# Kernel tuning notes

Hardware: AMD Instinct MI355X
Metric: run time of the kernel (lower is better)

## Reference

```python
import jax, jax.numpy as jnp
import numpy as np

VOCAB = 32000
D_IN = 1024      # == 2 * N_OUT so highway uses raw x (k=3 SRU path)
N_OUT = 512      # hidden per direction
N_LAYERS = 4
L, B = 1024, 16


def _sru_bidir_layer(x, W, b, n):
    """x: (L,B,2n), W: (2n, 6n) [dir0: xt,f,r | dir1: xt,f,r], b: (4n,) = [bf(2n), br(2n)]."""
    u = jnp.einsum('lbd,dk->lbk', x, W)  # (L,B,6n)
    bf, br = b[:2 * n], b[2 * n:]
    hs, cs = [], []
    for d, rev in ((0, False), (1, True)):
        ud = u[..., d * 3 * n:(d + 1) * 3 * n]
        xt = ud[..., :n]
        f = jax.nn.sigmoid(ud[..., n:2 * n] + bf[d * n:(d + 1) * n])
        r = jax.nn.sigmoid(ud[..., 2 * n:3 * n] + br[d * n:(d + 1) * n])
        xp = x[..., d * n:(d + 1) * n]  # highway input (k=3 case)

        def step(c, inp):
            xt_t, f_t, r_t, xp_t = inp
            c = f_t * c + (1.0 - f_t) * xt_t
            h = r_t * jnp.tanh(c) + (1.0 - r_t) * xp_t
            return c, h

        c0 = jnp.zeros((x.shape[1], n), x.dtype)
        c_last, h = jax.lax.scan(step, c0, (xt, f, r, xp), reverse=rev)
        hs.append(h)
        cs.append(c_last)
    return jnp.concatenate(hs, -1), jnp.concatenate(cs, -1)


def setup_inputs() -> dict:
    key = jax.random.key(0)
    k1, k2, k3, k4 = jax.random.split(key, 4)
    rnn_input = jax.random.randint(k1, (L, B), 0, VOCAB, dtype=jnp.int32)
    input_lengths = jax.random.randint(k2, (B,), 1, L + 1, dtype=jnp.int32)
    emb = jax.random.normal(k3, (VOCAB, D_IN), dtype=jnp.float32) * 0.05
    scale = 1.0 / np.sqrt(D_IN)
    Ws = jax.random.normal(k4, (N_LAYERS, D_IN, 6 * N_OUT), dtype=jnp.float32) * scale
    bs = jnp.zeros((N_LAYERS, 4 * N_OUT), dtype=jnp.float32)
    return {"rnn_input": rnn_input, "input_lengths": input_lengths,
            "emb": emb, "Ws": Ws, "bs": bs}


def reference(rnn_input, input_lengths, emb, Ws, bs):
    # input_lengths is unused in the original forward (no packing applied to SRU input)
    n = Ws.shape[-1] // 6
    x = emb[rnn_input]  # (L,B,D_IN)
    c_finals = []
    for l in range(Ws.shape[0]):
        x, c = _sru_bidir_layer(x, Ws[l], bs[l], n)
        c_finals.append(c)
    hidden = jnp.stack(c_finals, 0)  # (N_LAYERS, B, 2n)
    return x, hidden
```

## Files before the change

kernel.cpp:

```cpp
#include <hip/hip_runtime.h>
#include <hip/hip_bf16.h>
#include <cmath>

#define L_SEQ  1024
#define BATCH  16
#define NOUT   512
#define DIN    1024
#define NBIG   3072
#define NLAYERS 4
#define NTOK   (L_SEQ * BATCH)
#define NCHAIN 16384
#define SEG    32
#define SEGLEN (L_SEQ / SEG)

typedef __attribute__((ext_vector_type(8))) short bf16x8;
typedef __attribute__((ext_vector_type(4))) float f32x4;

__device__ __forceinline__ unsigned short f2bf(float f) {
    unsigned x = __float_as_uint(f);
    unsigned r = (x + 0x7fffu + ((x >> 16) & 1u)) >> 16;
    return (unsigned short)r;
}
__device__ __forceinline__ float bf2f(unsigned short hv) {
    return __uint_as_float((unsigned)hv << 16);
}
__device__ __forceinline__ float sigmf(float v) {
    return 1.f / (1.f + __expf(-v));
}
__device__ __forceinline__ void async16(const void* g, const void* l) {
    __builtin_amdgcn_global_load_lds(
        (const __attribute__((address_space(1))) unsigned int*)g,
        (__attribute__((address_space(3))) unsigned int*)l, 16, 0, 0);
}

__global__ __launch_bounds__(256)
void transpose_w(const float* __restrict__ Ws, unsigned short* __restrict__ Wt) {
    __shared__ float tile[32][33];
    int l = blockIdx.z;
    const float* W = Ws + (size_t)l * DIN * NBIG;
    unsigned short* Wo = Wt + (size_t)l * NBIG * DIN;
    int n0 = blockIdx.x * 32, k0 = blockIdx.y * 32;
    int tx = threadIdx.x & 31, ty = threadIdx.x >> 5;
    #pragma unroll
    for (int i = 0; i < 4; i++)
        tile[ty + 8 * i][tx] = W[(size_t)(k0 + ty + 8 * i) * NBIG + n0 + tx];
    __syncthreads();
    #pragma unroll
    for (int i = 0; i < 4; i++)
        Wo[(size_t)(n0 + ty + 8 * i) * DIN + k0 + tx] = f2bf(tile[tx][ty + 8 * i]);
}

__global__ void embed_kernel(const int* __restrict__ tok,
                             const float* __restrict__ emb,
                             float* __restrict__ x,
                             unsigned short* __restrict__ xbf) {
    int t = blockIdx.x;
    int row = tok[t];
    float4 v = ((const float4*)(emb + (size_t)row * DIN))[threadIdx.x];
    ((float4*)(x + (size_t)t * DIN))[threadIdx.x] = v;
    ushort4 h;
    h.x = f2bf(v.x); h.y = f2bf(v.y); h.z = f2bf(v.z); h.w = f2bf(v.w);
    ((ushort4*)(xbf + (size_t)t * DIN))[threadIdx.x] = h;
}


#define STAGE_A(b, mh, kt, src)                                             \
    do {                                                                    \
        _Pragma("unroll")                                                   \
        for (int q = 0; q < 2; q++) {                                       \
            int rbase = q * 128 + (mh) * 64 + w * 8;                        \
            async16((src) + (size_t)(rbase + sr) * DIN + (kt) * 64 + sc * 8,\
                    &lds[b][0][rbase * 64]);                                \
        }                                                                   \
    } while (0)

#define STAGE_B(b, nh, kt, src)                                             \
    do {                                                                    \
        _Pragma("unroll")                                                   \
        for (int q = 0; q < 2; q++) {                                       \
            int gi = q * 8 + w;                                             \
            int rbase = (gi >> 2) * 64 + (nh) * 32 + (gi & 3) * 8;          \
            async16((src) + (size_t)(rbase + sr) * DIN + (kt) * 64 + sc * 8,\
                    &lds[b][1][rbase * 64]);                                \
        }                                                                   \
    } while (0)

#define LOAD_A(b, mh)                                                       \
    do {                                                                    \
        _Pragma("unroll")                                                   \
        for (int i = 0; i < 4; i++) {                                       \
            int ra = wm * 128 + (mh) * 64 + i * 16 + l16;                   \
            _Pragma("unroll")                                               \
            for (int kk = 0; kk < 2; kk++) {                                \
                int slot = (kk * 4 + quad) ^ (ra & 7);                      \
                af[i][kk] = *(const bf16x8*)&lds[b][0][ra * 64 + slot * 8]; \
            }                                                               \
        }                                                                   \
    } while (0)

#define LOAD_B(b, nh)                                                       \
    do {                                                                    \
        _Pragma("unroll")                                                   \
        for (int j = 0; j < 2; j++) {                                       \
            int rb = wn * 64 + (nh) * 32 + j * 16 + l16;                    \
            _Pragma("unroll")                                               \
            for (int kk = 0; kk < 2; kk++) {                                \
                int slot = (kk * 4 + quad) ^ (rb & 7);                      \
                bg[nh][j][kk] = *(const bf16x8*)&lds[b][1][rb * 64 + slot * 8]; \
            }                                                               \
        }                                                                   \
    } while (0)

#define MMA(mh, nh)                                                         \
    do {                                                                    \
        __builtin_amdgcn_s_setprio(1);                                      \
        _Pragma("unroll")                                                   \
        for (int i = 0; i < 4; i++)                                         \
            _Pragma("unroll")                                               \
            for (int j = 0; j < 2; j++)                                     \
                _Pragma("unroll")                                           \
                for (int kk = 0; kk < 2; kk++)                              \
                    acc[(mh) * 4 + i][(nh) * 2 + j] =                       \
                        __builtin_amdgcn_mfma_f32_16x16x32_bf16(            \
                            af[i][kk], bg[nh][j][kk],                       \
                            acc[(mh) * 4 + i][(nh) * 2 + j], 0, 0, 0);      \
        __builtin_amdgcn_s_setprio(0);                                      \
    } while (0)

#define BAR()   __builtin_amdgcn_s_barrier()
#define LGKM0() do { asm volatile("s_waitcnt lgkmcnt(0)" ::: "memory");     \
                     __builtin_amdgcn_sched_barrier(0); } while (0)
#define LGKM8() asm volatile("s_waitcnt lgkmcnt(8)" ::: "memory")
#define VM6()   asm volatile("s_waitcnt vmcnt(6)" ::: "memory")
#define VM0()   asm volatile("s_waitcnt vmcnt(0)" ::: "memory")

__global__ __launch_bounds__(512)
void gemm_bf16(const unsigned short* __restrict__ Abf,
               const unsigned short* __restrict__ Bt,
               unsigned short* __restrict__ u_xt,
               unsigned short* __restrict__ u_f,
               unsigned short* __restrict__ u_r) {
    __shared__ __align__(16) unsigned short lds[2][2][256 * 64];

    const int tid  = threadIdx.x;
    const int lane = tid & 63;
    const int w    = tid >> 6;
    const int wm   = w >> 2, wn = w & 3;
    const int quad = lane >> 4, l16 = lane & 15;

    const int flat = blockIdx.y * (NBIG / 256) + blockIdx.x;
    const int swz  = (flat & 7) * (NTOK / 256 * NBIG / 256 / 8) + (flat >> 3);
    const int M0 = (swz / (NBIG / 256)) * 256;
    const int N0 = (swz % (NBIG / 256)) * 256;

    const unsigned short* Asrc = Abf + (size_t)M0 * DIN;
    const unsigned short* Bsrc = Bt  + (size_t)N0 * DIN;

    f32x4 acc[8][4];
    #pragma unroll
    for (int i = 0; i < 8; i++)
        #pragma unroll
        for (int j = 0; j < 4; j++)
            acc[i][j] = (f32x4){0.f, 0.f, 0.f, 0.f};

    const int sr = lane >> 3;
    const int sc = (lane & 7) ^ sr;

    bf16x8 af[4][2], bg[2][2][2];

    STAGE_A(0, 0, 0, Asrc); STAGE_B(0, 0, 0, Bsrc);
    STAGE_B(0, 1, 0, Bsrc); STAGE_A(0, 1, 0, Asrc);
    STAGE_A(1, 0, 1, Asrc); STAGE_B(1, 1, 1, Bsrc); STAGE_A(1, 1, 1, Asrc);
    VM6();
    BAR();

    const int NITER = DIN / 128;
    for (int t = 0; t < NITER; t++) {
        const int k1 = 2 * t + 1;
        const bool more = (t < NITER - 1);

        LOAD_A(0, 0); LOAD_B(0, 0);
        STAGE_B(1, 0, k1, Bsrc);
        LGKM8(); BAR(); LGKM0(); MMA(0, 0); BAR();
        LOAD_B(0, 1);
        if (more) STAGE_A(0, 0, k1 + 1, Asrc);
        BAR(); LGKM0(); MMA(0, 1); BAR();
        LOAD_A(0, 1);
        if (more) STAGE_B(0, 1, k1 + 1, Bsrc);
        BAR(); LGKM0(); MMA(1, 1); BAR();
        if (more) { STAGE_A(0, 1, k1 + 1, Asrc); VM6(); }
        else      { VM0(); }
        BAR(); MMA(1, 0); BAR();

        LOAD_A(1, 0); LOAD_B(1, 0);
        if (more) STAGE_B(0, 0, k1 + 1, Bsrc);
        LGKM8(); BAR(); LGKM0(); MMA(0, 0); BAR();
        LOAD_B(1, 1);
        if (more) STAGE_A(1, 0, k1 + 2, Asrc);
        BAR(); LGKM0(); MMA(0, 1); BAR();
        LOAD_A(1, 1);
        if (more) STAGE_B(1, 1, k1 + 2, Bsrc);
        BAR(); LGKM0(); MMA(1, 1); BAR();
        if (more) { STAGE_A(1, 1, k1 + 2, Asrc); VM6(); }
        BAR(); MMA(1, 0); BAR();
    }

    #pragma unroll
    for (int i = 0; i < 8; i++) {
        int gm = M0 + wm * 128 + i * 16 + quad * 4;
        #pragma unroll
        for (int j = 0; j < 4; j++) {
            int gn = N0 + wn * 64 + j * 16 + l16;
            int dir  = gn >= 3 * NOUT;
            int jj   = gn - dir * 3 * NOUT;
            int plane = jj >> 9;
            int feat  = jj & 511;
            unsigned short* p = (plane == 0 ? u_xt : plane == 1 ? u_f : u_r)
                                + (size_t)gm * DIN + dir * NOUT + feat;
            #pragma unroll
            for (int r = 0; r < 4; r++) p[(size_t)r * DIN] = f2bf(acc[i][j][r]);
        }
    }
}


__global__ __launch_bounds__(256)
void scan_phaseA(const unsigned short* __restrict__ u_xt, const unsigned short* __restrict__ u_f,
                 const float* __restrict__ bias,
                 float* __restrict__ Aseg, float* __restrict__ Bseg) {
    int hgl = blockIdx.x * 256 + threadIdx.x;
    int c2 = hgl & (NCHAIN / 2 - 1);
    int s = hgl >> 13;
    int chain = c2 * 2;
    int rest = chain & 1023;
    float bf0 = bias[rest], bf1 = bias[rest + 1];

    int d = rest >> 9;
    int t0 = d ? (L_SEQ - 1 - s * SEGLEN) : (s * SEGLEN);
    int sgn = d ? -1 : 1;
    long long idx = (long long)t0 * NCHAIN + chain;
    long long step = (long long)sgn * NCHAIN;

    float c0 = 0.f, A0 = 1.f, c1 = 0.f, A1 = 1.f;
    #pragma unroll 8
    for (int j = 0; j < SEGLEN; j++) {
        unsigned xt2 = *(const unsigned*)(u_xt + idx);
        unsigned f2v = *(const unsigned*)(u_f + idx);
        float xt0 = bf2f((unsigned short)xt2), xt1 = bf2f((unsigned short)(xt2 >> 16));
        float f0 = sigmf(bf2f((unsigned short)f2v) + bf0);
        float f1 = sigmf(bf2f((unsigned short)(f2v >> 16)) + bf1);
        c0 = f0 * c0 + (1.f - f0) * xt0;  A0 *= f0;
        c1 = f1 * c1 + (1.f - f1) * xt1;  A1 *= f1;
        idx += step;
    }
    int g = s * NCHAIN + chain;
    *(float2*)(Aseg + g) = make_float2(A0, A1);
    *(float2*)(Bseg + g) = make_float2(c0, c1);
}

__global__ __launch_bounds__(256)
void scan_phaseB(const float* __restrict__ Aseg, const float* __restrict__ Bseg,
                 float* __restrict__ cstart, float* __restrict__ c_out) {
    int chain = blockIdx.x * 256 + threadIdx.x;
    float c = 0.f;
    #pragma unroll
    for (int s = 0; s < SEG; s++) {
        int g = s * NCHAIN + chain;
        cstart[g] = c;
        c = Aseg[g] * c + Bseg[g];
    }
    c_out[chain] = c;
}

__global__ __launch_bounds__(256)
void scan_phaseC(const unsigned short* __restrict__ u_xt, const unsigned short* __restrict__ u_f,
                 const unsigned short* __restrict__ u_r,
                 float* __restrict__ x, unsigned short* __restrict__ xbf,
                 const float* __restrict__ bias, const float* __restrict__ cstart,
                 int write_bf) {
    int hgl = blockIdx.x * 256 + threadIdx.x;
    int c2 = hgl & (NCHAIN / 2 - 1);
    int s = hgl >> 13;
    int chain = c2 * 2;
    int rest = chain & 1023;
    float bf0 = bias[rest],        bf1 = bias[rest + 1];
    float br0 = bias[1024 + rest], br1 = bias[1024 + rest + 1];

    int d = rest >> 9;
    int t0 = d ? (L_SEQ - 1 - s * SEGLEN) : (s * SEGLEN);
    int sgn = d ? -1 : 1;
    long long idx = (long long)t0 * NCHAIN + chain;
    long long step = (long long)sgn * NCHAIN;

    float2 cs = *(const float2*)(cstart + (size_t)s * NCHAIN + chain);
    float c0 = cs.x, c1 = cs.y;
    #pragma unroll 4
    for (int j = 0; j < SEGLEN; j++) {
        unsigned xt2 = *(const unsigned*)(u_xt + idx);
        unsigned f2v = *(const unsigned*)(u_f + idx);
        unsigned r2v = *(const unsigned*)(u_r + idx);
        float2 xp = *(const float2*)(x + idx);
        float f0 = sigmf(bf2f((unsigned short)f2v) + bf0);
        float f1 = sigmf(bf2f((unsigned short)(f2v >> 16)) + bf1);
        float r0 = sigmf(bf2f((unsigned short)r2v) + br0);
        float r1 = sigmf(bf2f((unsigned short)(r2v >> 16)) + br1);
        c0 = f0 * c0 + (1.f - f0) * bf2f((unsigned short)xt2);
        c1 = f1 * c1 + (1.f - f1) * bf2f((unsigned short)(xt2 >> 16));
        float th0 = 1.f - 2.f / (__expf(2.f * c0) + 1.f);
        float th1 = 1.f - 2.f / (__expf(2.f * c1) + 1.f);
        float h0 = r0 * th0 + (1.f - r0) * xp.x;
        float h1 = r1 * th1 + (1.f - r1) * xp.y;
        *(float2*)(x + idx) = make_float2(h0, h1);
        if (write_bf)
            *(unsigned*)(xbf + idx) = (unsigned)f2bf(h0) | ((unsigned)f2bf(h1) << 16);
        idx += step;
    }
}

extern "C" void kernel_launch(void* const* d_in, const int* in_sizes, int n_in,
                              void* d_out, int out_size, void* d_ws, size_t ws_size,
                              hipStream_t stream) {
    const int*   tok = (const int*)d_in[0];
    const float* emb = (const float*)d_in[2];
    const float* Ws  = (const float*)d_in[3];
    const float* bs  = (const float*)d_in[4];

    float* out    = (float*)d_out;
    float* x      = out;
    float* hidden = out + (size_t)NTOK * DIN;

    char* ws = (char*)d_ws;
    unsigned short* u_xt   = (unsigned short*)ws;
    unsigned short* u_f    = (unsigned short*)(ws + (32u  << 20));
    unsigned short* u_r    = (unsigned short*)(ws + (64u  << 20));
    unsigned short* xbf    = (unsigned short*)(ws + (96u  << 20));
    unsigned short* Wt     = (unsigned short*)(ws + (128u << 20));
    float*          Aseg   = (float*)(ws + (152u << 20));
    float*          Bseg   = (float*)(ws + (154u << 20));
    float*          cstart = (float*)(ws + (156u << 20));

    transpose_w<<<dim3(NBIG / 32, DIN / 32, NLAYERS), 256, 0, stream>>>(Ws, Wt);
    embed_kernel<<<NTOK, 256, 0, stream>>>(tok, emb, x, xbf);

    const int scan_blocks2 = NCHAIN * SEG / 2 / 256;

    for (int l = 0; l < NLAYERS; l++) {
        const unsigned short* Wl = Wt + (size_t)l * NBIG * DIN;
        const float* b = bs + (size_t)l * 4 * NOUT;
        gemm_bf16<<<dim3(NBIG / 256, NTOK / 256), 512, 0, stream>>>(xbf, Wl, u_xt, u_f, u_r);
        scan_phaseA<<<scan_blocks2, 256, 0, stream>>>(u_xt, u_f, b, Aseg, Bseg);
        scan_phaseB<<<NCHAIN / 256, 256, 0, stream>>>(Aseg, Bseg, cstart,
                                                      hidden + (size_t)l * BATCH * DIN);
        scan_phaseC<<<scan_blocks2, 256, 0, stream>>>(u_xt, u_f, u_r, x, xbf, b, cstart,
                                                      l < NLAYERS - 1);
    }
}
```

Before: 913.3 us.

## Stage GEMM epilogue through LDS for 16-byte stores; widen scan kernels to 4 chains

The GEMM epilogue now writes accumulators as bf16 into LDS with an XOR swizzle, then reads them back as 8-element vectors. It writes those to global memory as coalesced 16-byte stores, replacing scattered 2-byte strided stores. Because a 256-wide N tile never crosses a 512-feature plane boundary, the plane pointer is computed once per block. The scan phase A and C kernels now handle 4 chains per thread with 8/16-byte loads, and phase B handles 2 chains per thread, which cuts thread count and widens memory accesses but lowers parallelism and raises register use.

Result: no change. 907.7 us (-0.6%).

```diff
diff --git a/kernel.cpp b/kernel.cpp
--- a/kernel.cpp
+++ b/kernel.cpp
@@ -141,6 +141,7 @@
                unsigned short* __restrict__ u_f,
                unsigned short* __restrict__ u_r) {
     __shared__ __align__(16) unsigned short lds[2][2][256 * 64];
+    unsigned short* Cbuf = &lds[0][0][0];
 
     const int tid  = threadIdx.x;
     const int lane = tid & 63;
@@ -155,6 +156,12 @@
 
     const unsigned short* Asrc = Abf + (size_t)M0 * DIN;
     const unsigned short* Bsrc = Bt  + (size_t)N0 * DIN;
+
+    const int dir   = N0 >= 3 * NOUT;
+    const int jj0   = N0 - dir * 3 * NOUT;
+    const int plane = jj0 >> 9;
+    unsigned short* pl = (plane == 0 ? u_xt : plane == 1 ? u_f : u_r)
+                         + dir * NOUT + (jj0 & 511);
 
     f32x4 acc[8][4];
     #pragma unroll
@@ -206,20 +213,29 @@
     }
 
     #pragma unroll
-    for (int i = 0; i < 8; i++) {
-        int gm = M0 + wm * 128 + i * 16 + quad * 4;
+    for (int i = 0; i < 8; i++)
         #pragma unroll
-        for (int j = 0; j < 4; j++) {
-            int gn = N0 + wn * 64 + j * 16 + l16;
-            int dir  = gn >= 3 * NOUT;
-            int jj   = gn - dir * 3 * NOUT;
-            int plane = jj >> 9;
-            int feat  = jj & 511;
-            unsigned short* p = (plane == 0 ? u_xt : plane == 1 ? u_f : u_r)
-                                + (size_t)gm * DIN + dir * NOUT + feat;
+        for (int j = 0; j < 4; j++)
             #pragma unroll
-            for (int r = 0; r < 4; r++) p[(size_t)r * DIN] = f2bf(acc[i][j][r]);
-        }
+            for (int r = 0; r < 4; r++) {
+                int row = wm * 128 + i * 16 + quad * 4 + r;
+                int ft  = (wn * 64 + j * 16 + l16) ^ (quad << 4);
+                Cbuf[row * 256 + ft] = f2bf(acc[i][j][r]);
+            }
+    asm volatile("s_waitcnt lgkmcnt(0)" ::: "memory");
+    BAR();
+    bf16x8 ctmp[16];
+    #pragma unroll
+    for (int ps = 0; ps < 16; ps++) {
+        int cg = ps * 512 + tid; int row = cg >> 5; int c0 = cg & 31;
+        int st = row * 256 + ((c0 << 3) ^ (((row >> 2) & 3) << 4));
+        ctmp[ps] = *(const bf16x8*)&Cbuf[st];
+    }
+    LGKM0();
+    #pragma unroll
+    for (int ps = 0; ps < 16; ps++) {
+        int cg = ps * 512 + tid; int row = cg >> 5; int c0 = cg & 31;
+        *(bf16x8*)(pl + (size_t)(M0 + row) * DIN + c0 * 8) = ctmp[ps];
     }
 }
 
@@ -229,11 +245,13 @@
                  const float* __restrict__ bias,
                  float* __restrict__ Aseg, float* __restrict__ Bseg) {
     int hgl = blockIdx.x * 256 + threadIdx.x;
-    int c2 = hgl & (NCHAIN / 2 - 1);
-    int s = hgl >> 13;
-    int chain = c2 * 2;
+    int c4 = hgl & (NCHAIN / 4 - 1);
+    int s = hgl >> 12;
+    int chain = c4 * 4;
     int rest = chain & 1023;
-    float bf0 = bias[rest], bf1 = bias[rest + 1];
+    float bf[4];
+    #pragma unroll
+    for (int v = 0; v < 4; v++) bf[v] = bias[rest + v];
 
     int d = rest >> 9;
     int t0 = d ? (L_SEQ - 1 - s * SEGLEN) : (s * SEGLEN);
@@ -241,35 +259,42 @@
     long long idx = (long long)t0 * NCHAIN + chain;
     long long step = (long long)sgn * NCHAIN;
 
-    float c0 = 0.f, A0 = 1.f, c1 = 0.f, A1 = 1.f;
-    #pragma unroll 8
+    float c[4] = {0.f, 0.f, 0.f, 0.f}, A[4] = {1.f, 1.f, 1.f, 1.f};
+    #pragma unroll 4
     for (int j = 0; j < SEGLEN; j++) {
-        unsigned xt2 = *(const unsigned*)(u_xt + idx);
-        unsigned f2v = *(const unsigned*)(u_f + idx);
-        float xt0 = bf2f((unsigned short)xt2), xt1 = bf2f((unsigned short)(xt2 >> 16));
-        float f0 = sigmf(bf2f((unsigned short)f2v) + bf0);
-        float f1 = sigmf(bf2f((unsigned short)(f2v >> 16)) + bf1);
-        c0 = f0 * c0 + (1.f - f0) * xt0;  A0 *= f0;
-        c1 = f1 * c1 + (1.f - f1) * xt1;  A1 *= f1;
+        uint2 xt4 = *(const uint2*)(u_xt + idx);
+        uint2 f4  = *(const uint2*)(u_f + idx);
+        #pragma unroll
+        for (int v = 0; v < 4; v++) {
+            unsigned xw = (v < 2) ? xt4.x : xt4.y;
+            unsigned fw = (v < 2) ? f4.x : f4.y;
+            float xt = bf2f((unsigned short)(xw >> ((v & 1) * 16)));
+            float f  = sigmf(bf2f((unsigned short)(fw >> ((v & 1) * 16))) + bf[v]);
+            c[v] = f * c[v] + (1.f - f) * xt;
+            A[v] *= f;
+        }
         idx += step;
     }
     int g = s * NCHAIN + chain;
-    *(float2*)(Aseg + g) = make_float2(A0, A1);
-    *(float2*)(Bseg + g) = make_float2(c0, c1);
+    *(float4*)(Aseg + g) = make_float4(A[0], A[1], A[2], A[3]);
+    *(float4*)(Bseg + g) = make_float4(c[0], c[1], c[2], c[3]);
 }
 
 __global__ __launch_bounds__(256)
 void scan_phaseB(const float* __restrict__ Aseg, const float* __restrict__ Bseg,
                  float* __restrict__ cstart, float* __restrict__ c_out) {
-    int chain = blockIdx.x * 256 + threadIdx.x;
-    float c = 0.f;
+    int c2 = (blockIdx.x * 256 + threadIdx.x) * 2;
+    float cx = 0.f, cy = 0.f;
     #pragma unroll
     for (int s = 0; s < SEG; s++) {
-        int g = s * NCHAIN + chain;
-        cstart[g] = c;
-        c = Aseg[g] * c + Bseg[g];
-    }
-    c_out[chain] = c;
+        int g = s * NCHAIN + c2;
+        float2 A = *(const float2*)(Aseg + g);
+        float2 B = *(const float2*)(Bseg + g);
+        *(float2*)(cstart + g) = make_float2(cx, cy);
+        cx = A.x * cx + B.x;
+        cy = A.y * cy + B.y;
+    }
+    *(float2*)(c_out + c2) = make_float2(cx, cy);
 }
 
 __global__ __launch_bounds__(256)
@@ -279,12 +304,13 @@
                  const float* __restrict__ bias, const float* __restrict__ cstart,
                  int write_bf) {
     int hgl = blockIdx.x * 256 + threadIdx.x;
-    int c2 = hgl & (NCHAIN / 2 - 1);
-    int s = hgl >> 13;
-    int chain = c2 * 2;
+    int c4 = hgl & (NCHAIN / 4 - 1);
+    int s = hgl >> 12;
+    int chain = c4 * 4;
     int rest = chain & 1023;
-    float bf0 = bias[rest],        bf1 = bias[rest + 1];
-    float br0 = bias[1024 + rest], br1 = bias[1024 + rest + 1];
+    float bf[4], br[4];
+    #pragma unroll
+    for (int v = 0; v < 4; v++) { bf[v] = bias[rest + v]; br[v] = bias[1024 + rest + v]; }
 
     int d = rest >> 9;
     int t0 = d ? (L_SEQ - 1 - s * SEGLEN) : (s * SEGLEN);
@@ -292,27 +318,34 @@
     long long idx = (long long)t0 * NCHAIN + chain;
     long long step = (long long)sgn * NCHAIN;
 
-    float2 cs = *(const float2*)(cstart + (size_t)s * NCHAIN + chain);
-    float c0 = cs.x, c1 = cs.y;
-    #pragma unroll 4
+    float4 cs = *(const float4*)(cstart + (size_t)s * NCHAIN + chain);
+    float c[4] = {cs.x, cs.y, cs.z, cs.w};
+    #pragma unroll 2
     for (int j = 0; j < SEGLEN; j++) {
-        unsigned xt2 = *(const unsigned*)(u_xt + idx);
-        unsigned f2v = *(const unsigned*)(u_f + idx);
-        unsigned r2v = *(const unsigned*)(u_r + idx);
-        float2 xp = *(const float2*)(x + idx);
-        float f0 = sigmf(bf2f((unsigned short)f2v) + bf0);
-        float f1 = sigmf(bf2f((unsigned short)(f2v >> 16)) + bf1);
-        float r0 = sigmf(bf2f((unsigned short)r2v) + br0);
-        float r1 = sigmf(bf2f((unsigned short)(r2v >> 16)) + br1);
-        c0 = f0 * c0 + (1.f - f0) * bf2f((unsigned short)xt2);
-        c1 = f1 * c1 + (1.f - f1) * bf2f((unsigned short)(xt2 >> 16));
-        float th0 = 1.f - 2.f / (__expf(2.f * c0) + 1.f);
-        float th1 = 1.f - 2.f / (__expf(2.f * c1) + 1.f);
-        float h0 = r0 * th0 + (1.f - r0) * xp.x;
-        float h1 = r1 * th1 + (1.f - r1) * xp.y;
-        *(float2*)(x + idx) = make_float2(h0, h1);
-        if (write_bf)
-            *(unsigned*)(xbf + idx) = (unsigned)f2bf(h0) | ((unsigned)f2bf(h1) << 16);
+        uint2 xt4 = *(const uint2*)(u_xt + idx);
+        uint2 f4  = *(const uint2*)(u_f + idx);
+        uint2 r4  = *(const uint2*)(u_r + idx);
+        float4 xp = *(const float4*)(x + idx);
+        float h[4];
+        #pragma unroll
+        for (int v = 0; v < 4; v++) {
+            unsigned xw = (v < 2) ? xt4.x : xt4.y;
+            unsigned fw = (v < 2) ? f4.x : f4.y;
+            unsigned rw = (v < 2) ? r4.x : r4.y;
+            float xpv = (v == 0) ? xp.x : (v == 1) ? xp.y : (v == 2) ? xp.z : xp.w;
+            float f = sigmf(bf2f((unsigned short)(fw >> ((v & 1) * 16))) + bf[v]);
+            float r = sigmf(bf2f((unsigned short)(rw >> ((v & 1) * 16))) + br[v]);
+            c[v] = f * c[v] + (1.f - f) * bf2f((unsigned short)(xw >> ((v & 1) * 16)));
+            float th = 1.f - 2.f / (__expf(2.f * c[v]) + 1.f);
+            h[v] = r * th + (1.f - r) * xpv;
+        }
+        *(float4*)(x + idx) = make_float4(h[0], h[1], h[2], h[3]);
+        if (write_bf) {
+            uint2 hb;
+            hb.x = (unsigned)f2bf(h[0]) | ((unsigned)f2bf(h[1]) << 16);
+            hb.y = (unsigned)f2bf(h[2]) | ((unsigned)f2bf(h[3]) << 16);
+            *(uint2*)(xbf + idx) = hb;
+        }
         idx += step;
     }
 }
@@ -342,16 +375,16 @@
     transpose_w<<<dim3(NBIG / 32, DIN / 32, NLAYERS), 256, 0, stream>>>(Ws, Wt);
     embed_kernel<<<NTOK, 256, 0, stream>>>(tok, emb, x, xbf);
 
-    const int scan_blocks2 = NCHAIN * SEG / 2 / 256;
+    const int scan_blocks4 = NCHAIN * SEG / 4 / 256;
 
     for (int l = 0; l < NLAYERS; l++) {
         const unsigned short* Wl = Wt + (size_t)l * NBIG * DIN;
         const float* b = bs + (size_t)l * 4 * NOUT;
         gemm_bf16<<<dim3(NBIG / 256, NTOK / 256), 512, 0, stream>>>(xbf, Wl, u_xt, u_f, u_r);
-        scan_phaseA<<<scan_blocks2, 256, 0, stream>>>(u_xt, u_f, b, Aseg, Bseg);
-        scan_phaseB<<<NCHAIN / 256, 256, 0, stream>>>(Aseg, Bseg, cstart,
-                                                      hidden + (size_t)l * BATCH * DIN);
-        scan_phaseC<<<scan_blocks2, 256, 0, stream>>>(u_xt, u_f, u_r, x, xbf, b, cstart,
+        scan_phaseA<<<scan_blocks4, 256, 0, stream>>>(u_xt, u_f, b, Aseg, Bseg);
+        scan_phaseB<<<NCHAIN / 2 / 256, 256, 0, stream>>>(Aseg, Bseg, cstart,
+                                                          hidden + (size_t)l * BATCH * DIN);
+        scan_phaseC<<<scan_blocks4, 256, 0, stream>>>(u_xt, u_f, u_r, x, xbf, b, cstart,
                                                       l < NLAYERS - 1);
     }
 }
```
